# Kernel tuning notes

Measured on AMD Instinct MI355X. Metric: run time of the kernel, lower is better.

## Reference

```python
import jax, jax.numpy as jnp
import numpy as np

TBL_V = 1000      # table_id_vocab
IDX_V = 100000    # idx_id_vocab
D     = 128       # embed_dim
T_OUT = 8         # output_length
BLK   = 2048      # block_size
H     = 8         # n_heads
L     = 2         # n_layers
DFF   = 2048      # nn.TransformerEncoderLayer default dim_feedforward
HID   = 4 * D     # hidden_dim
B, S  = 128, 200
NSEG  = IDX_V // BLK + 1   # 49 segment tables
EPS   = 1e-5


def setup_inputs() -> dict:
    key = jax.random.key(0)
    ks = iter(jax.random.split(key, 48))
    def n(shape, s=0.02):
        return jax.random.normal(next(ks), shape, jnp.float32) * s
    return {
        "table_id_seq": jax.random.randint(next(ks), (B, S), 0, TBL_V, jnp.int32),
        "idx_id_seq":   jax.random.randint(next(ks), (B, S), 0, IDX_V, jnp.int32),
        # embedding tables (idx tables stacked: segment s occupies rows [s*BLK,(s+1)*BLK))
        "table_embed": n((TBL_V, D), 1.0),
        "idx_embed":   n((NSEG * BLK, D), 1.0),
        # two independent TransformerEncoders (axis 0: 0=table, 1=idx), L layers each
        "Wqkv": n((2, L, 3 * D, D)), "bqkv": jnp.zeros((2, L, 3 * D), jnp.float32),
        "Wo":   n((2, L, D, D)),     "bo":   jnp.zeros((2, L, D), jnp.float32),
        "ln1_g": jnp.ones((2, L, D), jnp.float32), "ln1_b": jnp.zeros((2, L, D), jnp.float32),
        "W1": n((2, L, DFF, D)), "b1": jnp.zeros((2, L, DFF), jnp.float32),
        "W2": n((2, L, D, DFF)), "b2": jnp.zeros((2, L, D), jnp.float32),
        "ln2_g": jnp.ones((2, L, D), jnp.float32), "ln2_b": jnp.zeros((2, L, D), jnp.float32),
        "Wlin": n((HID, 2 * D)), "blin": jnp.zeros((HID,), jnp.float32),
        "Wtab": n((TBL_V, HID + 1)), "btab": jnp.zeros((TBL_V,), jnp.float32),
        "Widx": n((IDX_V, HID + 1)), "bidx": jnp.zeros((IDX_V,), jnp.float32),
    }


def _ln(x, g, b):
    m = x.mean(-1, keepdims=True)
    v = ((x - m) ** 2).mean(-1, keepdims=True)
    return (x - m) / jnp.sqrt(v + EPS) * g + b


def _encoder(x, p):
    """Post-norm TransformerEncoder (PyTorch defaults, eval mode). x: [B,S,D]."""
    Wqkv, bqkv, Wo, bo, g1, be1, W1, bf1, W2, bf2, g2, be2 = p
    Bz, Sl, Dm = x.shape
    hd = Dm // H
    for l in range(L):
        qkv = x @ Wqkv[l].T + bqkv[l]
        q, k, v = jnp.split(qkv, 3, axis=-1)
        q = q.reshape(Bz, Sl, H, hd)
        k = k.reshape(Bz, Sl, H, hd)
        v = v.reshape(Bz, Sl, H, hd)
        att = jnp.einsum('bqhd,bkhd->bhqk', q, k) * (hd ** -0.5)
        att = jax.nn.softmax(att, axis=-1)
        o = jnp.einsum('bhqk,bkhd->bqhd', att, v).reshape(Bz, Sl, Dm)
        o = o @ Wo[l].T + bo[l]
        x = _ln(x + o, g1[l], be1[l])
        f = jax.nn.relu(x @ W1[l].T + bf1[l]) @ W2[l].T + bf2[l]
        x = _ln(x + f, g2[l], be2[l])
    return x


def reference(table_id_seq, idx_id_seq, table_embed, idx_embed,
              Wqkv, bqkv, Wo, bo, ln1_g, ln1_b, W1, b1, W2, b2, ln2_g, ln2_b,
              Wlin, blin, Wtab, btab, Widx, bidx):
    enc_p = (Wqkv, bqkv, Wo, bo, ln1_g, ln1_b, W1, b1, W2, b2, ln2_g, ln2_b)
    te = table_embed[table_id_seq]                    # [B,S,D]
    # segment-routed lookup: row (seg*BLK + local) of stacked tables == original id
    ie = idx_embed[idx_id_seq]                        # [B,S,D]
    te = _encoder(te, tuple(a[0] for a in enc_p))
    ie = _encoder(ie, tuple(a[1] for a in enc_p))
    h = jnp.concatenate([te.mean(axis=1), ie.mean(axis=1)], axis=-1)  # mean over seq
    h = jax.nn.relu(h @ Wlin.T + blin)                # [B,HID]
    t = jnp.arange(T_OUT, dtype=h.dtype)
    # projection of [hidden, t]: base term + t * (last weight column)
    tab = (h @ Wtab[:, :HID].T + btab)[:, None, :] + t[None, :, None] * Wtab[:, HID][None, None, :]
    idx = (h @ Widx[:, :HID].T + bidx)[:, None, :] + t[None, :, None] * Widx[:, HID][None, None, :]
    return tab.reshape(-1, TBL_V), idx.reshape(-1, IDX_V)
```

## Files before the change

kernel.cpp:

```cpp
#include <hip/hip_runtime.h>

typedef __bf16 bf16x8 __attribute__((ext_vector_type(8)));
typedef float floatx4 __attribute__((ext_vector_type(4)));

__device__ __forceinline__ float u2f(unsigned short u) {
  union { unsigned int i; float f; } v; v.i = ((unsigned int)u) << 16; return v.f;
}
__device__ __forceinline__ unsigned short f2b(float f) {
  union { float f; unsigned int i; } v; v.f = f;
  unsigned int r = (v.i + 0x7fffu + ((v.i >> 16) & 1u)) >> 16;
  return (unsigned short)r;
}

__device__ __forceinline__ void gl16(const void* g, void* l) {
  __builtin_amdgcn_global_load_lds(
      (const __attribute__((address_space(1))) unsigned int*)g,
      (__attribute__((address_space(3))) unsigned int*)l, 16, 0, 0);
}

#define LDS_STRIDE 48

__global__ __launch_bounds__(256) void gemm_kernel(
    const unsigned short* __restrict__ A, int lda,
    const float* __restrict__ W, int ldw,
    const float* __restrict__ bias,
    unsigned short* __restrict__ outB, float* __restrict__ outF,
    int M, int N, int K, int ldc, int mode)
{
  __shared__ unsigned short As[128 * LDS_STRIDE];
  __shared__ unsigned short Bs[128 * LDS_STRIDE];

  const int tid  = threadIdx.x;
  const int m0   = blockIdx.y * 128;
  const int n0   = blockIdx.x * 128;
  const int wave = tid >> 6;
  const int lane = tid & 63;
  const int wm   = (wave >> 1) * 64;
  const int wn   = (wave & 1) * 64;
  const int lr   = lane & 15;
  const int lq   = lane >> 4;

  floatx4 acc[4][4];
#pragma unroll
  for (int i = 0; i < 4; i++)
#pragma unroll
    for (int j = 0; j < 4; j++)
      acc[i][j] = (floatx4){0.f, 0.f, 0.f, 0.f};

  for (int k0 = 0; k0 < K; k0 += 32) {
    __syncthreads();
#pragma unroll
    for (int i = 0; i < 2; i++) {
      int c   = tid + i * 256;
      int row = c >> 2;
      int k8  = (c & 3) * 8;
      uint4 val = {0u, 0u, 0u, 0u};
      if (m0 + row < M)
        val = *(const uint4*)(A + (size_t)(m0 + row) * lda + k0 + k8);
      *(uint4*)(&As[row * LDS_STRIDE + k8]) = val;
    }
#pragma unroll
    for (int i = 0; i < 4; i++) {
      int c   = tid + i * 256;
      int row = c >> 3;
      int k4  = (c & 7) * 4;
      float f0 = 0.f, f1 = 0.f, f2 = 0.f, f3 = 0.f;
      if (n0 + row < N) {
        const float* p = W + (size_t)(n0 + row) * ldw + k0 + k4;
        f0 = p[0]; f1 = p[1]; f2 = p[2]; f3 = p[3];
      }
      ushort4 pk;
      pk.x = f2b(f0); pk.y = f2b(f1); pk.z = f2b(f2); pk.w = f2b(f3);
      *(ushort4*)(&Bs[row * LDS_STRIDE + k4]) = pk;
    }
    __syncthreads();

    bf16x8 af[4], bfr[4];
#pragma unroll
    for (int t = 0; t < 4; t++) {
      af[t]  = *(const bf16x8*)(&As[(wm + t * 16 + lr) * LDS_STRIDE + lq * 8]);
      bfr[t] = *(const bf16x8*)(&Bs[(wn + t * 16 + lr) * LDS_STRIDE + lq * 8]);
    }
#pragma unroll
    for (int tm = 0; tm < 4; tm++)
#pragma unroll
      for (int tn = 0; tn < 4; tn++)
        acc[tm][tn] = __builtin_amdgcn_mfma_f32_16x16x32_bf16(
            af[tm], bfr[tn], acc[tm][tn], 0, 0, 0);
  }

#pragma unroll
  for (int tm = 0; tm < 4; tm++) {
#pragma unroll
    for (int tn = 0; tn < 4; tn++) {
      int gcol = n0 + wn + tn * 16 + lr;
      if (gcol >= N) continue;
      float bs = bias[gcol];
      if (mode == 2) {
        float wl = W[(size_t)gcol * ldw + K];
#pragma unroll
        for (int r = 0; r < 4; r++) {
          int grow = m0 + wm + tm * 16 + lq * 4 + r;
          float base = acc[tm][tn][r] + bs;
          float* op = outF + ((size_t)grow * 8) * (size_t)N + gcol;
#pragma unroll
          for (int t = 0; t < 8; t++)
            op[(size_t)t * N] = base + (float)t * wl;
        }
      } else {
#pragma unroll
        for (int r = 0; r < 4; r++) {
          int grow = m0 + wm + tm * 16 + lq * 4 + r;
          if (grow < M) {
            float v = acc[tm][tn][r] + bs;
            if (mode == 1) v = fmaxf(v, 0.f);
            outB[(size_t)grow * ldc + gcol] = f2b(v);
          }
        }
      }
    }
  }
}

#define QKSTR 40
#define PSTR  232

__global__ __launch_bounds__(256) void attn_kernel(
    const unsigned short* __restrict__ qkv, unsigned short* __restrict__ out)
{
  __shared__ __attribute__((aligned(16))) unsigned short qsh[208 * QKSTR];
  __shared__ __attribute__((aligned(16))) unsigned short ksh[208 * QKSTR];
  __shared__ __attribute__((aligned(16))) unsigned short vsh[16 * PSTR];
  __shared__ __attribute__((aligned(16))) unsigned short psh[4][16 * PSTR];

  const int bh   = blockIdx.x;
  const int b    = bh >> 3, h = bh & 7;
  const int tid  = threadIdx.x;
  const int wave = tid >> 6;
  const int lane = tid & 63;
  const int lr   = lane & 15;
  const int lq   = lane >> 4;
  const size_t rowbase = (size_t)b * 200;

  for (int i = tid; i < 208 * QKSTR / 2; i += 256) {
    ((unsigned int*)qsh)[i] = 0u;
    ((unsigned int*)ksh)[i] = 0u;
  }
  for (int i = tid; i < 16 * PSTR / 2; i += 256)
    ((unsigned int*)vsh)[i] = 0u;
  for (int i = tid; i < 4 * 16 * PSTR / 2; i += 256)
    ((unsigned int*)&psh[0][0])[i] = 0u;
  __syncthreads();

  for (int i = tid; i < 800; i += 256) {
    int s = i >> 2, d4 = (i & 3) * 4;
    const unsigned short* base = qkv + (rowbase + s) * 384 + h * 16 + d4;
    uint2 qv = *(const uint2*)(base);
    uint2 kv = *(const uint2*)(base + 128);
    uint2 vv = *(const uint2*)(base + 256);
    *(uint2*)&qsh[s * QKSTR + d4] = qv;
    *(uint2*)&ksh[s * QKSTR + d4] = kv;
    vsh[(d4 + 0) * PSTR + s] = (unsigned short)(vv.x & 0xffffu);
    vsh[(d4 + 1) * PSTR + s] = (unsigned short)(vv.x >> 16);
    vsh[(d4 + 2) * PSTR + s] = (unsigned short)(vv.y & 0xffffu);
    vsh[(d4 + 3) * PSTR + s] = (unsigned short)(vv.y >> 16);
  }
  __syncthreads();

  unsigned short* pw = &psh[wave][0];

  for (int t = wave; t < 13; t += 4) {
    const int q0 = t * 16;
    bf16x8 qf = *(const bf16x8*)&qsh[(q0 + lr) * QKSTR + lq * 8];

    floatx4 s[13];
#pragma unroll
    for (int c = 0; c < 13; c++) {
      bf16x8 kf = *(const bf16x8*)&ksh[(c * 16 + lr) * QKSTR + lq * 8];
      s[c] = __builtin_amdgcn_mfma_f32_16x16x32_bf16(
          qf, kf, (floatx4){0.f, 0.f, 0.f, 0.f}, 0, 0, 0);
    }

    float mx[4] = {-1e30f, -1e30f, -1e30f, -1e30f};
#pragma unroll
    for (int c = 0; c < 13; c++)
#pragma unroll
      for (int r = 0; r < 4; r++) {
        float v = s[c][r] * 0.25f;
        if (c == 12 && lr >= 8) v = -1e30f;
        s[c][r] = v;
        mx[r] = fmaxf(mx[r], v);
      }
#pragma unroll
    for (int m = 1; m < 16; m <<= 1)
#pragma unroll
      for (int r = 0; r < 4; r++)
        mx[r] = fmaxf(mx[r], __shfl_xor(mx[r], m, 16));

    float sm[4] = {0.f, 0.f, 0.f, 0.f};
#pragma unroll
    for (int c = 0; c < 13; c++)
#pragma unroll
      for (int r = 0; r < 4; r++) {
        float e = __expf(s[c][r] - mx[r]);
        s[c][r] = e;
        sm[r] += e;
      }
#pragma unroll
    for (int m = 1; m < 16; m <<= 1)
#pragma unroll
      for (int r = 0; r < 4; r++)
        sm[r] += __shfl_xor(sm[r], m, 16);

#pragma unroll
    for (int c = 0; c < 13; c++)
#pragma unroll
      for (int r = 0; r < 4; r++)
        pw[(lq * 4 + r) * PSTR + c * 16 + lr] = f2b(s[c][r]);

    floatx4 o = {0.f, 0.f, 0.f, 0.f};
#pragma unroll
    for (int ks = 0; ks < 7; ks++) {
      bf16x8 pf = *(const bf16x8*)&pw[lr * PSTR + ks * 32 + lq * 8];
      bf16x8 vf = *(const bf16x8*)&vsh[lr * PSTR + ks * 32 + lq * 8];
      o = __builtin_amdgcn_mfma_f32_16x16x32_bf16(pf, vf, o, 0, 0, 0);
    }

#pragma unroll
    for (int r = 0; r < 4; r++) {
      int q = q0 + lq * 4 + r;
      if (q < 200)
        out[(rowbase + q) * 128 + h * 16 + lr] = f2b(o[r] / sm[r]);
    }
  }
}

#define CHIM 18048

__global__ __launch_bounds__(256) void prep_kernel(
    const float* __restrict__ W1, const float* __restrict__ b1,
    const float* __restrict__ W2, unsigned short* __restrict__ img)
{
  const int blk = blockIdx.x;
  const int pi  = blk >> 5, c = blk & 31;
  const int tid = threadIdx.x;
  unsigned short* o = img + (size_t)blk * CHIM;
  const float* w1 = W1 + ((size_t)pi * 2048 + c * 64) * 128;
  const float* w2 = W2 + (size_t)pi * 128 * 2048 + c * 64;

  for (int u = tid; u < 64 * 34; u += 256) {
    int row = u / 34, c4 = (u % 34) * 4;
    ushort4 pk = {0, 0, 0, 0};
    if (c4 < 128) {
      const float* p = w1 + row * 128 + c4;
      pk.x = f2b(p[0]); pk.y = f2b(p[1]); pk.z = f2b(p[2]); pk.w = f2b(p[3]);
    }
    *(ushort4*)&o[row * 136 + c4] = pk;
  }
  for (int u = tid; u < 128 * 18; u += 256) {
    int row = u / 18, c4 = (u % 18) * 4;
    ushort4 pk = {0, 0, 0, 0};
    if (c4 < 64) {
      const float* p = w2 + (size_t)row * 2048 + c4;
      pk.x = f2b(p[0]); pk.y = f2b(p[1]); pk.z = f2b(p[2]); pk.w = f2b(p[3]);
    }
    *(ushort4*)&o[8704 + row * 72 + c4] = pk;
  }
  if (tid < 64)
    ((float*)(o + 17920))[tid] = b1[(size_t)pi * 2048 + c * 64 + tid];
}

__global__ __launch_bounds__(256) void ffn_kernel(
    const unsigned short* __restrict__ x,
    const unsigned short* __restrict__ wimg,
    const float* __restrict__ b2,
    unsigned short* __restrict__ out)
{
  __shared__ __attribute__((aligned(16))) unsigned short wbuf[2][CHIM];
  __shared__ __attribute__((aligned(16))) unsigned short mids[64 * 72];

  const int tid  = threadIdx.x;
  const int wave = tid >> 6;
  const int lane = tid & 63;
  const int lr   = lane & 15;
  const int lq   = lane >> 4;
  const int m0   = blockIdx.x * 64;
  const int wm   = wave * 16;

  bf16x8 af[4];
#pragma unroll
  for (int ks = 0; ks < 4; ks++)
    af[ks] = *(const bf16x8*)(x + (size_t)(m0 + wm + lr) * 128 + ks * 32 + lq * 8);

  floatx4 acc[8];
#pragma unroll
  for (int i = 0; i < 8; i++) acc[i] = (floatx4){0.f, 0.f, 0.f, 0.f};

  {
    const unsigned short* src = wimg;
#pragma unroll
    for (int i = 0; i < 9; i++) {
      int u = tid + i * 256;
      if (u < 2256) gl16(src + (size_t)u * 8, &wbuf[0][(size_t)u * 8]);
    }
  }

  for (int c = 0; c < 32; c++) {
    if (c + 1 < 32) {
      const unsigned short* src = wimg + (size_t)(c + 1) * CHIM;
      unsigned short* dst = &wbuf[(c + 1) & 1][0];
#pragma unroll
      for (int i = 0; i < 9; i++) {
        int u = tid + i * 256;
        if (u < 2256) gl16(src + (size_t)u * 8, dst + (size_t)u * 8);
      }
      asm volatile("s_waitcnt vmcnt(9)" ::: "memory");
    } else {
      asm volatile("s_waitcnt vmcnt(0)" ::: "memory");
    }
    __builtin_amdgcn_s_barrier();
    __builtin_amdgcn_sched_barrier(0);

    const unsigned short* wb = &wbuf[c & 1][0];

    floatx4 macc[4];
#pragma unroll
    for (int tn = 0; tn < 4; tn++) macc[tn] = (floatx4){0.f, 0.f, 0.f, 0.f};
#pragma unroll
    for (int ks = 0; ks < 4; ks++)
#pragma unroll
      for (int tn = 0; tn < 4; tn++) {
        bf16x8 wf = *(const bf16x8*)&wb[(tn * 16 + lr) * 136 + ks * 32 + lq * 8];
        macc[tn] = __builtin_amdgcn_mfma_f32_16x16x32_bf16(af[ks], wf, macc[tn], 0, 0, 0);
      }
    const float* b1c = (const float*)(wb + 17920);
#pragma unroll
    for (int tn = 0; tn < 4; tn++) {
      float bb = b1c[tn * 16 + lr];
#pragma unroll
      for (int r = 0; r < 4; r++) {
        float v = fmaxf(macc[tn][r] + bb, 0.f);
        mids[(wm + lq * 4 + r) * 72 + tn * 16 + lr] = f2b(v);
      }
    }
#pragma unroll
    for (int ks = 0; ks < 2; ks++) {
      bf16x8 mf = *(const bf16x8*)&mids[(wm + lr) * 72 + ks * 32 + lq * 8];
#pragma unroll
      for (int tn = 0; tn < 8; tn++) {
        bf16x8 wf = *(const bf16x8*)&wb[8704 + (tn * 16 + lr) * 72 + ks * 32 + lq * 8];
        acc[tn] = __builtin_amdgcn_mfma_f32_16x16x32_bf16(mf, wf, acc[tn], 0, 0, 0);
      }
    }
    __builtin_amdgcn_s_barrier();
  }

#pragma unroll
  for (int tn = 0; tn < 8; tn++) {
    float bb = b2[tn * 16 + lr];
#pragma unroll
    for (int r = 0; r < 4; r++) {
      int row = m0 + wm + lq * 4 + r;
      out[(size_t)row * 128 + tn * 16 + lr] = f2b(acc[tn][r] + bb);
    }
  }
}

__global__ __launch_bounds__(256) void ln_kernel(
    unsigned short* __restrict__ x, const unsigned short* __restrict__ sub,
    const float* __restrict__ g, const float* __restrict__ b)
{
  int row  = blockIdx.x * 4 + (threadIdx.x >> 6);
  int lane = threadIdx.x & 63;
  size_t base = (size_t)row * 128;
  int d0 = lane * 2, d1 = d0 + 1;
  float v0 = u2f(x[base + d0]) + u2f(sub[base + d0]);
  float v1 = u2f(x[base + d1]) + u2f(sub[base + d1]);
  float s  = v0 + v1;
  float ss = v0 * v0 + v1 * v1;
  for (int m = 1; m < 64; m <<= 1) {
    s  += __shfl_xor(s, m, 64);
    ss += __shfl_xor(ss, m, 64);
  }
  float mean = s * (1.f / 128.f);
  float var  = ss * (1.f / 128.f) - mean * mean;
  float r    = rsqrtf(var + 1e-5f);
  x[base + d0] = f2b((v0 - mean) * r * g[d0] + b[d0]);
  x[base + d1] = f2b((v1 - mean) * r * g[d1] + b[d1]);
}

__global__ __launch_bounds__(128) void gather_kernel(
    const int* __restrict__ ids, const float* __restrict__ table,
    unsigned short* __restrict__ x)
{
  int rid = blockIdx.x;
  int d   = threadIdx.x;
  int id  = ids[rid];
  x[(size_t)rid * 128 + d] = f2b(table[(size_t)id * 128 + d]);
}

__global__ __launch_bounds__(128) void pool_kernel(
    const unsigned short* __restrict__ x, unsigned short* __restrict__ hcat,
    int col0)
{
  int b = blockIdx.x;
  int d = threadIdx.x;
  float s = 0.f;
  for (int t = 0; t < 200; t++)
    s += u2f(x[(size_t)(b * 200 + t) * 128 + d]);
  hcat[b * 256 + col0 + d] = f2b(s * (1.f / 200.f));
}

static void gemm(hipStream_t st, const unsigned short* A, int lda,
                 const float* W, int ldw, const float* bias,
                 unsigned short* outB, float* outF,
                 int M, int N, int K, int ldc, int mode)
{
  dim3 grid((N + 127) / 128, (M + 127) / 128);
  gemm_kernel<<<grid, dim3(256), 0, st>>>(A, lda, W, ldw, bias, outB, outF,
                                          M, N, K, ldc, mode);
}

extern "C" void kernel_launch(void* const* d_in, const int* in_sizes, int n_in,
                              void* d_out, int out_size, void* d_ws, size_t ws_size,
                              hipStream_t stream)
{
  const int*   tab_ids     = (const int*)d_in[0];
  const int*   idx_ids     = (const int*)d_in[1];
  const float* table_embed = (const float*)d_in[2];
  const float* idx_embed   = (const float*)d_in[3];
  const float* Wqkv = (const float*)d_in[4];
  const float* bqkv = (const float*)d_in[5];
  const float* Wo   = (const float*)d_in[6];
  const float* bo   = (const float*)d_in[7];
  const float* ln1g = (const float*)d_in[8];
  const float* ln1b = (const float*)d_in[9];
  const float* W1   = (const float*)d_in[10];
  const float* b1   = (const float*)d_in[11];
  const float* W2   = (const float*)d_in[12];
  const float* b2   = (const float*)d_in[13];
  const float* ln2g = (const float*)d_in[14];
  const float* ln2b = (const float*)d_in[15];
  const float* Wlin = (const float*)d_in[16];
  const float* blin = (const float*)d_in[17];
  const float* Wtab = (const float*)d_in[18];
  const float* btab = (const float*)d_in[19];
  const float* Widx = (const float*)d_in[20];
  const float* bidx = (const float*)d_in[21];
  float* out = (float*)d_out;
  char*  ws  = (char*)d_ws;

  const size_t off_x    = 0;
  const size_t off_qkv  = 6553600;
  const size_t off_attn = 26214400;
  const size_t off_hcat = 32768000;
  const size_t off_h    = off_hcat + 65536;
  const size_t off_wimg = 33030144;

  unsigned short* x    = (unsigned short*)(ws + off_x);
  unsigned short* qkv  = (unsigned short*)(ws + off_qkv);
  unsigned short* o2   = qkv;
  unsigned short* attn = (unsigned short*)(ws + off_attn);
  unsigned short* hcat = (unsigned short*)(ws + off_hcat);
  unsigned short* h    = (unsigned short*)(ws + off_h);
  unsigned short* wimg = (unsigned short*)(ws + off_wimg);

  prep_kernel<<<128, 256, 0, stream>>>(W1, b1, W2, wimg);

  for (int e = 0; e < 2; e++) {
    gather_kernel<<<25600, 128, 0, stream>>>(
        e == 0 ? tab_ids : idx_ids,
        e == 0 ? table_embed : idx_embed, x);
    for (int l = 0; l < 2; l++) {
      int pi = e * 2 + l;
      gemm(stream, x, 128, Wqkv + (size_t)pi * 384 * 128, 128,
           bqkv + (size_t)pi * 384, qkv, nullptr, 25600, 384, 128, 384, 0);
      attn_kernel<<<1024, 256, 0, stream>>>(qkv, attn);
      gemm(stream, attn, 128, Wo + (size_t)pi * 128 * 128, 128,
           bo + (size_t)pi * 128, o2, nullptr, 25600, 128, 128, 128, 0);
      ln_kernel<<<6400, 256, 0, stream>>>(x, o2, ln1g + pi * 128, ln1b + pi * 128);
      ffn_kernel<<<400, 256, 0, stream>>>(
          x, wimg + (size_t)pi * 32 * CHIM, b2 + pi * 128, o2);
      ln_kernel<<<6400, 256, 0, stream>>>(x, o2, ln2g + pi * 128, ln2b + pi * 128);
    }
    pool_kernel<<<128, 128, 0, stream>>>(x, hcat, e * 128);
  }

  gemm(stream, hcat, 256, Wlin, 256, blin, h, nullptr, 128, 512, 256, 512, 1);
  gemm(stream, h, 512, Wtab, 513, btab, nullptr, out,           128, 1000,   512, 1000,   2);
  gemm(stream, h, 512, Widx, 513, bidx, nullptr, out + 1024000, 128, 100000, 512, 100000, 2);
}
```

Measured before the change: 1.557 ms.

## Fuse Wo and FFN GEMMs with residual LayerNorm and add a prepacked QKV kernel

Converts the QKV and Wo weights, together with their biases and LN1 parameters, once into bf16 LDS-ready images inside the prep kernel. It replaces the generic GEMM for QKV with a specialised double-buffered kernel. The Wo GEMM and the FFN now apply the residual add and LayerNorm in their epilogues, so the separate LN kernels and the intermediate buffer round trips go away. The gather and pool kernels are also reworked to do more work per thread and to split the sequence reduction across more threads. The cost is more complex epilogues, higher register pressure from holding full-row values, and in-place updates of x.

Result: faster. 1.296 ms (-16.8%).

```diff
diff --git a/kernel.cpp b/kernel.cpp
--- a/kernel.cpp
+++ b/kernel.cpp
@@ -17,6 +17,10 @@
       (const __attribute__((address_space(1))) unsigned int*)g,
       (__attribute__((address_space(3))) unsigned int*)l, 16, 0, 0);
 }
+
+#define FCH 18048
+#define QCH 8832
+#define OCH 18176
 
 #define LDS_STRIDE 48
 
@@ -235,49 +239,85 @@
   }
 }
 
-#define CHIM 18048
-
 __global__ __launch_bounds__(256) void prep_kernel(
     const float* __restrict__ W1, const float* __restrict__ b1,
-    const float* __restrict__ W2, unsigned short* __restrict__ img)
+    const float* __restrict__ W2,
+    const float* __restrict__ Wqkv, const float* __restrict__ bqkv,
+    const float* __restrict__ Wo, const float* __restrict__ bo,
+    const float* __restrict__ ln1g, const float* __restrict__ ln1b,
+    unsigned short* __restrict__ fimg, unsigned short* __restrict__ qimg,
+    unsigned short* __restrict__ oimg)
 {
   const int blk = blockIdx.x;
-  const int pi  = blk >> 5, c = blk & 31;
   const int tid = threadIdx.x;
-  unsigned short* o = img + (size_t)blk * CHIM;
-  const float* w1 = W1 + ((size_t)pi * 2048 + c * 64) * 128;
-  const float* w2 = W2 + (size_t)pi * 128 * 2048 + c * 64;
-
-  for (int u = tid; u < 64 * 34; u += 256) {
-    int row = u / 34, c4 = (u % 34) * 4;
-    ushort4 pk = {0, 0, 0, 0};
-    if (c4 < 128) {
-      const float* p = w1 + row * 128 + c4;
-      pk.x = f2b(p[0]); pk.y = f2b(p[1]); pk.z = f2b(p[2]); pk.w = f2b(p[3]);
-    }
-    *(ushort4*)&o[row * 136 + c4] = pk;
-  }
-  for (int u = tid; u < 128 * 18; u += 256) {
-    int row = u / 18, c4 = (u % 18) * 4;
-    ushort4 pk = {0, 0, 0, 0};
-    if (c4 < 64) {
-      const float* p = w2 + (size_t)row * 2048 + c4;
-      pk.x = f2b(p[0]); pk.y = f2b(p[1]); pk.z = f2b(p[2]); pk.w = f2b(p[3]);
-    }
-    *(ushort4*)&o[8704 + row * 72 + c4] = pk;
-  }
-  if (tid < 64)
-    ((float*)(o + 17920))[tid] = b1[(size_t)pi * 2048 + c * 64 + tid];
-}
-
-__global__ __launch_bounds__(256) void ffn_kernel(
+  if (blk < 128) {
+    const int pi = blk >> 5, c = blk & 31;
+    unsigned short* o = fimg + (size_t)blk * FCH;
+    const float* w1 = W1 + ((size_t)pi * 2048 + c * 64) * 128;
+    const float* w2 = W2 + (size_t)pi * 128 * 2048 + c * 64;
+    for (int u = tid; u < 64 * 34; u += 256) {
+      int row = u / 34, c4 = (u % 34) * 4;
+      ushort4 pk = {0, 0, 0, 0};
+      if (c4 < 128) {
+        const float* p = w1 + row * 128 + c4;
+        pk.x = f2b(p[0]); pk.y = f2b(p[1]); pk.z = f2b(p[2]); pk.w = f2b(p[3]);
+      }
+      *(ushort4*)&o[row * 136 + c4] = pk;
+    }
+    for (int u = tid; u < 128 * 18; u += 256) {
+      int row = u / 18, c4 = (u % 18) * 4;
+      ushort4 pk = {0, 0, 0, 0};
+      if (c4 < 64) {
+        const float* p = w2 + (size_t)row * 2048 + c4;
+        pk.x = f2b(p[0]); pk.y = f2b(p[1]); pk.z = f2b(p[2]); pk.w = f2b(p[3]);
+      }
+      *(ushort4*)&o[8704 + row * 72 + c4] = pk;
+    }
+    if (tid < 64)
+      ((float*)(o + 17920))[tid] = b1[(size_t)pi * 2048 + c * 64 + tid];
+  } else if (blk < 152) {
+    const int q = blk - 128;
+    const int pi = q / 6, c = q % 6;
+    unsigned short* o = qimg + (size_t)q * QCH;
+    const float* w = Wqkv + ((size_t)pi * 384 + c * 64) * 128;
+    for (int u = tid; u < 64 * 34; u += 256) {
+      int row = u / 34, c4 = (u % 34) * 4;
+      ushort4 pk = {0, 0, 0, 0};
+      if (c4 < 128) {
+        const float* p = w + row * 128 + c4;
+        pk.x = f2b(p[0]); pk.y = f2b(p[1]); pk.z = f2b(p[2]); pk.w = f2b(p[3]);
+      }
+      *(ushort4*)&o[row * 136 + c4] = pk;
+    }
+    if (tid < 64)
+      ((float*)(o + 8704))[tid] = bqkv[(size_t)pi * 384 + c * 64 + tid];
+  } else {
+    const int pi = blk - 152;
+    unsigned short* o = oimg + (size_t)pi * OCH;
+    const float* w = Wo + (size_t)pi * 128 * 128;
+    for (int u = tid; u < 128 * 34; u += 256) {
+      int row = u / 34, c4 = (u % 34) * 4;
+      ushort4 pk = {0, 0, 0, 0};
+      if (c4 < 128) {
+        const float* p = w + row * 128 + c4;
+        pk.x = f2b(p[0]); pk.y = f2b(p[1]); pk.z = f2b(p[2]); pk.w = f2b(p[3]);
+      }
+      *(ushort4*)&o[row * 136 + c4] = pk;
+    }
+    if (tid < 128) {
+      ((float*)(o + 17408))[tid] = bo[(size_t)pi * 128 + tid];
+      ((float*)(o + 17664))[tid] = ln1g[(size_t)pi * 128 + tid];
+      ((float*)(o + 17920))[tid] = ln1b[(size_t)pi * 128 + tid];
+    }
+  }
+}
+
+__global__ __launch_bounds__(256) void qkv_kernel(
     const unsigned short* __restrict__ x,
     const unsigned short* __restrict__ wimg,
-    const float* __restrict__ b2,
     unsigned short* __restrict__ out)
 {
-  __shared__ __attribute__((aligned(16))) unsigned short wbuf[2][CHIM];
-  __shared__ __attribute__((aligned(16))) unsigned short mids[64 * 72];
+  __shared__ __attribute__((aligned(16))) unsigned short wbuf[2][QCH];
 
   const int tid  = threadIdx.x;
   const int wave = tid >> 6;
@@ -292,22 +332,175 @@
   for (int ks = 0; ks < 4; ks++)
     af[ks] = *(const bf16x8*)(x + (size_t)(m0 + wm + lr) * 128 + ks * 32 + lq * 8);
 
+#pragma unroll
+  for (int i = 0; i < 5; i++) {
+    int u = tid + i * 256;
+    if (u < 1104) gl16(wimg + (size_t)u * 8, &wbuf[0][(size_t)u * 8]);
+  }
+
+  for (int c = 0; c < 6; c++) {
+    if (c + 1 < 6) {
+      const unsigned short* src = wimg + (size_t)(c + 1) * QCH;
+      unsigned short* dst = &wbuf[(c + 1) & 1][0];
+#pragma unroll
+      for (int i = 0; i < 5; i++) {
+        int u = tid + i * 256;
+        if (u < 1104) gl16(src + (size_t)u * 8, dst + (size_t)u * 8);
+      }
+      asm volatile("s_waitcnt vmcnt(5)" ::: "memory");
+    } else {
+      asm volatile("s_waitcnt vmcnt(0)" ::: "memory");
+    }
+    __builtin_amdgcn_s_barrier();
+    __builtin_amdgcn_sched_barrier(0);
+
+    const unsigned short* wb = &wbuf[c & 1][0];
+
+    floatx4 acc[4];
+#pragma unroll
+    for (int tn = 0; tn < 4; tn++) acc[tn] = (floatx4){0.f, 0.f, 0.f, 0.f};
+#pragma unroll
+    for (int ks = 0; ks < 4; ks++)
+#pragma unroll
+      for (int tn = 0; tn < 4; tn++) {
+        bf16x8 wf = *(const bf16x8*)&wb[(tn * 16 + lr) * 136 + ks * 32 + lq * 8];
+        acc[tn] = __builtin_amdgcn_mfma_f32_16x16x32_bf16(af[ks], wf, acc[tn], 0, 0, 0);
+      }
+    const float* bc = (const float*)(wb + 8704);
+#pragma unroll
+    for (int tn = 0; tn < 4; tn++) {
+      float bb = bc[tn * 16 + lr];
+#pragma unroll
+      for (int r = 0; r < 4; r++) {
+        int row = m0 + wm + lq * 4 + r;
+        out[(size_t)row * 384 + c * 64 + tn * 16 + lr] = f2b(acc[tn][r] + bb);
+      }
+    }
+    __builtin_amdgcn_s_barrier();
+  }
+}
+
+__global__ __launch_bounds__(256) void wo_ln_kernel(
+    const unsigned short* __restrict__ attn,
+    const unsigned short* __restrict__ wimg,
+    unsigned short* __restrict__ x)
+{
+  __shared__ __attribute__((aligned(16))) unsigned short wbuf[OCH];
+
+  const int tid  = threadIdx.x;
+  const int wave = tid >> 6;
+  const int lane = tid & 63;
+  const int lr   = lane & 15;
+  const int lq   = lane >> 4;
+  const int m0   = blockIdx.x * 64;
+  const int wm   = wave * 16;
+
+#pragma unroll
+  for (int i = 0; i < 9; i++) {
+    int u = tid + i * 256;
+    if (u < 2272) gl16(wimg + (size_t)u * 8, &wbuf[(size_t)u * 8]);
+  }
+
+  bf16x8 af[4];
+#pragma unroll
+  for (int ks = 0; ks < 4; ks++)
+    af[ks] = *(const bf16x8*)(attn + (size_t)(m0 + wm + lr) * 128 + ks * 32 + lq * 8);
+
+  asm volatile("s_waitcnt vmcnt(0)" ::: "memory");
+  __builtin_amdgcn_s_barrier();
+  __builtin_amdgcn_sched_barrier(0);
+
   floatx4 acc[8];
 #pragma unroll
   for (int i = 0; i < 8; i++) acc[i] = (floatx4){0.f, 0.f, 0.f, 0.f};
-
-  {
-    const unsigned short* src = wimg;
-#pragma unroll
-    for (int i = 0; i < 9; i++) {
-      int u = tid + i * 256;
-      if (u < 2256) gl16(src + (size_t)u * 8, &wbuf[0][(size_t)u * 8]);
-    }
+#pragma unroll
+  for (int ks = 0; ks < 4; ks++)
+#pragma unroll
+    for (int tn = 0; tn < 8; tn++) {
+      bf16x8 wf = *(const bf16x8*)&wbuf[(tn * 16 + lr) * 136 + ks * 32 + lq * 8];
+      acc[tn] = __builtin_amdgcn_mfma_f32_16x16x32_bf16(af[ks], wf, acc[tn], 0, 0, 0);
+    }
+
+  const float* bo = (const float*)(wbuf + 17408);
+  const float* g  = (const float*)(wbuf + 17664);
+  const float* bb = (const float*)(wbuf + 17920);
+
+  float v[8][4];
+  float s[4] = {0.f, 0.f, 0.f, 0.f}, ss[4] = {0.f, 0.f, 0.f, 0.f};
+#pragma unroll
+  for (int tn = 0; tn < 8; tn++) {
+    float bsv = bo[tn * 16 + lr];
+#pragma unroll
+    for (int r = 0; r < 4; r++) {
+      size_t idx = (size_t)(m0 + wm + lq * 4 + r) * 128 + tn * 16 + lr;
+      float t = acc[tn][r] + bsv + u2f(x[idx]);
+      v[tn][r] = t;
+      s[r] += t;
+      ss[r] += t * t;
+    }
+  }
+#pragma unroll
+  for (int m = 1; m < 16; m <<= 1)
+#pragma unroll
+    for (int r = 0; r < 4; r++) {
+      s[r]  += __shfl_xor(s[r], m, 16);
+      ss[r] += __shfl_xor(ss[r], m, 16);
+    }
+  float mean[4], rstd[4];
+#pragma unroll
+  for (int r = 0; r < 4; r++) {
+    mean[r] = s[r] * (1.f / 128.f);
+    float var = ss[r] * (1.f / 128.f) - mean[r] * mean[r];
+    rstd[r] = rsqrtf(var + 1e-5f);
+  }
+#pragma unroll
+  for (int tn = 0; tn < 8; tn++) {
+    int col = tn * 16 + lr;
+    float gv = g[col], bv = bb[col];
+#pragma unroll
+    for (int r = 0; r < 4; r++) {
+      size_t idx = (size_t)(m0 + wm + lq * 4 + r) * 128 + col;
+      x[idx] = f2b((v[tn][r] - mean[r]) * rstd[r] * gv + bv);
+    }
+  }
+}
+
+__global__ __launch_bounds__(256) void ffn_kernel(
+    const unsigned short* __restrict__ xin,
+    const unsigned short* __restrict__ wimg,
+    const float* __restrict__ b2,
+    const float* __restrict__ g2, const float* __restrict__ bb2,
+    unsigned short* __restrict__ x)
+{
+  __shared__ __attribute__((aligned(16))) unsigned short wbuf[2][FCH];
+  __shared__ __attribute__((aligned(16))) unsigned short mids[64 * 72];
+
+  const int tid  = threadIdx.x;
+  const int wave = tid >> 6;
+  const int lane = tid & 63;
+  const int lr   = lane & 15;
+  const int lq   = lane >> 4;
+  const int m0   = blockIdx.x * 64;
+  const int wm   = wave * 16;
+
+  bf16x8 af[4];
+#pragma unroll
+  for (int ks = 0; ks < 4; ks++)
+    af[ks] = *(const bf16x8*)(xin + (size_t)(m0 + wm + lr) * 128 + ks * 32 + lq * 8);
+
+  floatx4 acc[8];
+#pragma unroll
+  for (int i = 0; i < 8; i++) acc[i] = (floatx4){0.f, 0.f, 0.f, 0.f};
+
+#pragma unroll
+  for (int i = 0; i < 9; i++) {
+    int u = tid + i * 256;
+    if (u < 2256) gl16(wimg + (size_t)u * 8, &wbuf[0][(size_t)u * 8]);
   }
 
   for (int c = 0; c < 32; c++) {
     if (c + 1 < 32) {
-      const unsigned short* src = wimg + (size_t)(c + 1) * CHIM;
+      const unsigned short* src = wimg + (size_t)(c + 1) * FCH;
       unsigned short* dst = &wbuf[(c + 1) & 1][0];
 #pragma unroll
       for (int i = 0; i < 9; i++) {
@@ -355,60 +548,79 @@
     __builtin_amdgcn_s_barrier();
   }
 
+  float v[8][4];
+  float s[4] = {0.f, 0.f, 0.f, 0.f}, ss[4] = {0.f, 0.f, 0.f, 0.f};
 #pragma unroll
   for (int tn = 0; tn < 8; tn++) {
-    float bb = b2[tn * 16 + lr];
+    float bsv = b2[tn * 16 + lr];
 #pragma unroll
     for (int r = 0; r < 4; r++) {
-      int row = m0 + wm + lq * 4 + r;
-      out[(size_t)row * 128 + tn * 16 + lr] = f2b(acc[tn][r] + bb);
-    }
-  }
-}
-
-__global__ __launch_bounds__(256) void ln_kernel(
-    unsigned short* __restrict__ x, const unsigned short* __restrict__ sub,
-    const float* __restrict__ g, const float* __restrict__ b)
-{
-  int row  = blockIdx.x * 4 + (threadIdx.x >> 6);
-  int lane = threadIdx.x & 63;
-  size_t base = (size_t)row * 128;
-  int d0 = lane * 2, d1 = d0 + 1;
-  float v0 = u2f(x[base + d0]) + u2f(sub[base + d0]);
-  float v1 = u2f(x[base + d1]) + u2f(sub[base + d1]);
-  float s  = v0 + v1;
-  float ss = v0 * v0 + v1 * v1;
-  for (int m = 1; m < 64; m <<= 1) {
-    s  += __shfl_xor(s, m, 64);
-    ss += __shfl_xor(ss, m, 64);
-  }
-  float mean = s * (1.f / 128.f);
-  float var  = ss * (1.f / 128.f) - mean * mean;
-  float r    = rsqrtf(var + 1e-5f);
-  x[base + d0] = f2b((v0 - mean) * r * g[d0] + b[d0]);
-  x[base + d1] = f2b((v1 - mean) * r * g[d1] + b[d1]);
-}
-
-__global__ __launch_bounds__(128) void gather_kernel(
+      size_t idx = (size_t)(m0 + wm + lq * 4 + r) * 128 + tn * 16 + lr;
+      float t = acc[tn][r] + bsv + u2f(x[idx]);
+      v[tn][r] = t;
+      s[r] += t;
+      ss[r] += t * t;
+    }
+  }
+#pragma unroll
+  for (int m = 1; m < 16; m <<= 1)
+#pragma unroll
+    for (int r = 0; r < 4; r++) {
+      s[r]  += __shfl_xor(s[r], m, 16);
+      ss[r] += __shfl_xor(ss[r], m, 16);
+    }
+  float mean[4], rstd[4];
+#pragma unroll
+  for (int r = 0; r < 4; r++) {
+    mean[r] = s[r] * (1.f / 128.f);
+    float var = ss[r] * (1.f / 128.f) - mean[r] * mean[r];
+    rstd[r] = rsqrtf(var + 1e-5f);
+  }
+#pragma unroll
+  for (int tn = 0; tn < 8; tn++) {
+    int col = tn * 16 + lr;
+    float gv = g2[col], bv = bb2[col];
+#pragma unroll
+    for (int r = 0; r < 4; r++) {
+      size_t idx = (size_t)(m0 + wm + lq * 4 + r) * 128 + col;
+      x[idx] = f2b((v[tn][r] - mean[r]) * rstd[r] * gv + bv);
+    }
+  }
+}
+
+__global__ __launch_bounds__(256) void gather_kernel(
     const int* __restrict__ ids, const float* __restrict__ table,
     unsigned short* __restrict__ x)
 {
-  int rid = blockIdx.x;
-  int d   = threadIdx.x;
-  int id  = ids[rid];
-  x[(size_t)rid * 128 + d] = f2b(table[(size_t)id * 128 + d]);
-}
-
-__global__ __launch_bounds__(128) void pool_kernel(
+  int t0 = blockIdx.x * 256 + threadIdx.x;
+#pragma unroll
+  for (int i = 0; i < 4; i++) {
+    int u = t0 + i * 409600;
+    int row = u >> 6, dp = (u & 63) << 1;
+    int id = ids[row];
+    const float* p = table + (size_t)id * 128 + dp;
+    float f0 = p[0], f1 = p[1];
+    ((unsigned int*)x)[u] = (unsigned int)f2b(f0) | ((unsigned int)f2b(f1) << 16);
+  }
+}
+
+__global__ __launch_bounds__(512) void pool_kernel(
     const unsigned short* __restrict__ x, unsigned short* __restrict__ hcat,
     int col0)
 {
+  __shared__ float part[512];
   int b = blockIdx.x;
-  int d = threadIdx.x;
+  int d = threadIdx.x & 127;
+  int g = threadIdx.x >> 7;
   float s = 0.f;
-  for (int t = 0; t < 200; t++)
-    s += u2f(x[(size_t)(b * 200 + t) * 128 + d]);
-  hcat[b * 256 + col0 + d] = f2b(s * (1.f / 200.f));
+  for (int t = 0; t < 50; t++)
+    s += u2f(x[(size_t)(b * 200 + g * 50 + t) * 128 + d]);
+  part[threadIdx.x] = s;
+  __syncthreads();
+  if (g == 0) {
+    float tot = part[d] + part[d + 128] + part[d + 256] + part[d + 384];
+    hcat[b * 256 + col0 + d] = f2b(tot * (1.f / 200.f));
+  }
 }
 
 static void gemm(hipStream_t st, const unsigned short* A, int lda,
@@ -455,35 +667,36 @@
   const size_t off_attn = 26214400;
   const size_t off_hcat = 32768000;
   const size_t off_h    = off_hcat + 65536;
-  const size_t off_wimg = 33030144;
+  const size_t off_fimg = 33030144;
+  const size_t off_qimg = off_fimg + (size_t)128 * FCH * 2;
+  const size_t off_oimg = off_qimg + (size_t)24 * QCH * 2;
 
   unsigned short* x    = (unsigned short*)(ws + off_x);
   unsigned short* qkv  = (unsigned short*)(ws + off_qkv);
-  unsigned short* o2   = qkv;
   unsigned short* attn = (unsigned short*)(ws + off_attn);
   unsigned short* hcat = (unsigned short*)(ws + off_hcat);
   unsigned short* h    = (unsigned short*)(ws + off_h);
-  unsigned short* wimg = (unsigned short*)(ws + off_wimg);
-
-  prep_kernel<<<128, 256, 0, stream>>>(W1, b1, W2, wimg);
+  unsigned short* fimg = (unsigned short*)(ws + off_fimg);
+  unsigned short* qimg = (unsigned short*)(ws + off_qimg);
+  unsigned short* oimg = (unsigned short*)(ws + off_oimg);
+
+  prep_kernel<<<156, 256, 0, stream>>>(W1, b1, W2, Wqkv, bqkv, Wo, bo,
+                                       ln1g, ln1b, fimg, qimg, oimg);
 
   for (int e = 0; e < 2; e++) {
-    gather_kernel<<<25600, 128, 0, stream>>>(
+    gather_kernel<<<1600, 256, 0, stream>>>(
         e == 0 ? tab_ids : idx_ids,
         e == 0 ? table_embed : idx_embed, x);
     for (int l = 0; l < 2; l++) {
       int pi = e * 2 + l;
-      gemm(stream, x, 128, Wqkv + (size_t)pi * 384 * 128, 128,
-           bqkv + (size_t)pi * 384, qkv, nullptr, 25600, 384, 128, 384, 0);
+      qkv_kernel<<<400, 256, 0, stream>>>(x, qimg + (size_t)pi * 6 * QCH, qkv);
       attn_kernel<<<1024, 256, 0, stream>>>(qkv, attn);
-      gemm(stream, attn, 128, Wo + (size_t)pi * 128 * 128, 128,
-           bo + (size_t)pi * 128, o2, nullptr, 25600, 128, 128, 128, 0);
-      ln_kernel<<<6400, 256, 0, stream>>>(x, o2, ln1g + pi * 128, ln1b + pi * 128);
+      wo_ln_kernel<<<400, 256, 0, stream>>>(attn, oimg + (size_t)pi * OCH, x);
       ffn_kernel<<<400, 256, 0, stream>>>(
-          x, wimg + (size_t)pi * 32 * CHIM, b2 + pi * 128, o2);
-      ln_kernel<<<6400, 256, 0, stream>>>(x, o2, ln2g + pi * 128, ln2b + pi * 128);
-    }
-    pool_kernel<<<128, 128, 0, stream>>>(x, hcat, e * 128);
+          x, fimg + (size_t)pi * 32 * FCH, b2 + pi * 128,
+          ln2g + pi * 128, ln2b + pi * 128, x);
+    }
+    pool_kernel<<<128, 512, 0, stream>>>(x, hcat, e * 128);
   }
 
   gemm(stream, hcat, 256, Wlin, 256, blin, h, nullptr, 128, 512, 256, 512, 1);
```
